# Performance work log

Hardware: AMD Instinct MI355X
Metric: run time of the kernel (lower is better)

Reference implementation:

```python
import jax, jax.numpy as jnp
import numpy as np

N_HEADS = 16
HEAD_DIM = 64
SEQ_LEN = 2048
BATCH = 1


def alibi_slopes(n_heads):
    start = 2.0 ** (-8.0 / n_heads)
    return jnp.asarray([start * start ** i for i in range(n_heads)], dtype=jnp.float32)


def setup_inputs() -> dict:
    key = jax.random.key(0)
    kq, kk, kv = jax.random.split(key, 3)
    shape = (BATCH, N_HEADS, SEQ_LEN, HEAD_DIM)
    return {
        "q": jax.random.normal(kq, shape, dtype=jnp.float32),
        "k": jax.random.normal(kk, shape, dtype=jnp.float32),
        "v": jax.random.normal(kv, shape, dtype=jnp.float32),
    }


def reference(q, k, v):
    # q,k,v: [B,H,S,D]
    seq_len = q.shape[2]
    head_dim = q.shape[3]
    scale = 1.0 / np.sqrt(head_dim).astype(np.float32)
    # scores: [B,H,S,S]
    scores = jnp.einsum("bhsd,bhtd->bhst", q, k) * scale
    pos = jnp.arange(seq_len)
    # distances[i, j] = j - i  (pos.unsqueeze(0) - pos.unsqueeze(1))
    distances = (pos[None, :] - pos[:, None]).astype(jnp.float32)  # [S,S]
    slopes = alibi_slopes(q.shape[1])  # [H]
    alibi = slopes[:, None, None] * distances[None, :, :]  # [H,S,S]
    scores = scores + alibi[None]
    attn = jax.nn.softmax(scores, axis=-1)
    return jnp.einsum("bhst,bhtd->bhsd", attn, v)
```

## Files before the change

### kernel.cpp

```cpp
#include <hip/hip_runtime.h>
#include <hip/hip_bf16.h>
#include <stdint.h>

#define N_HEADS 16
#define HEAD_DIM 64
#define SEQ_LEN 2048
#define KVBLK 32
#define NT 32
#define NTILE_TOT (SEQ_LEN / KVBLK)

typedef __bf16 bf16x8 __attribute__((ext_vector_type(8)));
typedef __bf16 bf16x4 __attribute__((ext_vector_type(4)));
typedef short  s16x4  __attribute__((ext_vector_type(4)));
typedef float  f32x4  __attribute__((ext_vector_type(4)));
typedef unsigned int u32x4 __attribute__((ext_vector_type(4)));

#if __has_builtin(__builtin_amdgcn_mfma_f32_16x16x16bf16_1k)
#define HAVE_MFMA16 1
#else
#define HAVE_MFMA16 0
#endif

static __device__ __forceinline__ unsigned pkbf(float a, float b) {
    union { __bf16 h[2]; unsigned u; } t;
    t.h[0] = (__bf16)a; t.h[1] = (__bf16)b;
    return t.u;
}

__global__ __launch_bounds__(256)
void prep_kernel(const float* __restrict__ k,
                 const float* __restrict__ v,
                 char* __restrict__ kimg,
                 char* __restrict__ vtimg) {
    const int ts  = blockIdx.x;
    const int h   = blockIdx.y;
    const int tid = threadIdx.x;
    const int s0  = ts * KVBLK;
    const size_t blk = ((size_t)h * NTILE_TOT + ts) * 4096;

    const int krow = tid >> 3;
    const int kcol = (tid & 7) * 8;
    const float* ks = k + ((size_t)h * SEQ_LEN + s0 + krow) * HEAD_DIM + kcol;
    f32x4 a = *(const f32x4*)ks;
    f32x4 b = *(const f32x4*)(ks + 4);
    bf16x8 kb;
    #pragma unroll
    for (int i = 0; i < 4; ++i) { kb[i] = (__bf16)a[i]; kb[4 + i] = (__bf16)b[i]; }
    *(bf16x8*)(kimg + blk + krow * 128 + ((kcol * 2) ^ ((krow & 7) << 4))) = kb;

    const int vc = tid & 63;
    const int vr = (tid >> 6) * 8;
    const float* vs = v + ((size_t)h * SEQ_LEN + s0 + vr) * HEAD_DIM + vc;
    bf16x8 vb;
    #pragma unroll
    for (int j = 0; j < 8; ++j) vb[j] = (__bf16)vs[(size_t)j * HEAD_DIM];
    *(bf16x8*)(vtimg + blk + (((vc * 64) + (vr * 2)) ^ ((vc & 7) << 4))) = vb;
}

template <bool IMG>
__global__ __launch_bounds__(512, 4)
void attn_alibi_kernel(const float* __restrict__ q,
                       const float* __restrict__ k,
                       const float* __restrict__ v,
                       float* __restrict__ out,
                       const char* __restrict__ kimg,
                       const char* __restrict__ vtimg) {
    const int tid  = threadIdx.x;
    const int wave = tid >> 6;
    const int lane = tid & 63;
    const int col  = lane & 15;
    const int g    = lane >> 4;
    const int half = wave >> 2;
    const int w4   = wave & 3;

    const int h      = blockIdx.y;
    const int qbase  = blockIdx.x * 64 + w4 * 16;
    const int kstart = half * (NT * KVBLK);

    const float* qh = q + (size_t)h * SEQ_LEN * HEAD_DIM;
    const float* kh = k + (size_t)h * SEQ_LEN * HEAD_DIM;
    const float* vh = v + (size_t)h * SEQ_LEN * HEAD_DIM;

    __shared__ alignas(16) char smem[32768];
    char* kbase  = smem + half * 8192;
    char* vtbase = smem + 16384 + half * 8192;

    const float LOG2E  = 1.4426950408889634f;
    const float scale2 = 0.125f * LOG2E;
    const float slope  = exp2f(-0.5f * (float)(h + 1));
    const float slope2 = slope * LOG2E;

    bf16x8 qf[2];
    {
        const float* qr = qh + (size_t)(qbase + col) * HEAD_DIM + g * 8;
        #pragma unroll
        for (int c = 0; c < 2; ++c)
            #pragma unroll
            for (int b = 0; b < 8; ++b) qf[c][b] = (__bf16)qr[c * 32 + b];
    }

    float cb[2][4];
    #pragma unroll
    for (int jt = 0; jt < 2; ++jt)
        #pragma unroll
        for (int r = 0; r < 4; ++r)
            cb[jt][r] = slope2 * (float)(jt * 16 + g * 4 + r - (qbase + col));

    float m = -1e30f, l = 0.0f;
    f32x4 acc[4];
    #pragma unroll
    for (int dt = 0; dt < 4; ++dt) acc[dt] = (f32x4)0.0f;

    const int hid  = tid & 255;
    const int krow = hid >> 3;
    const int kcol = (hid & 7) * 8;
    const int vc   = hid & 63;
    const int vr   = (hid >> 6) * 8;

    const char* kis = nullptr;
    const char* vis = nullptr;
    const float* ksrc = nullptr;
    const float* vsrc = nullptr;
    char* kdst  = nullptr;
    char* vtdst = nullptr;
    if constexpr (IMG) {
        const size_t base = ((size_t)h * NTILE_TOT + half * NT) * 4096 + hid * 16;
        kis = kimg + base;
        vis = vtimg + base;
        kdst  = kbase + hid * 16;
        vtdst = vtbase + hid * 16;
    } else {
        ksrc  = kh + (size_t)(kstart + krow) * HEAD_DIM + kcol;
        kdst  = kbase + krow * 128 + ((kcol * 2) ^ ((krow & 7) << 4));
        vsrc  = vh + (size_t)(kstart + vr) * HEAD_DIM + vc;
        vtdst = vtbase + (((vc * 64) + (vr * 2)) ^ ((vc & 7) << 4));
    }

    f32x4 kreg, vreg;
    f32x4 kr0, kr1;
    float vv[8];

    if constexpr (IMG) {
        kreg = *(const f32x4*)(kis);
        vreg = *(const f32x4*)(vis);
        *(f32x4*)(kdst)  = kreg;
        *(f32x4*)(vtdst) = vreg;
    } else {
        kr0 = *(const f32x4*)(ksrc);
        kr1 = *(const f32x4*)(ksrc + 4);
        #pragma unroll
        for (int j = 0; j < 8; ++j) vv[j] = vsrc[(size_t)j * HEAD_DIM];
        bf16x8 kb16, vb16;
        #pragma unroll
        for (int b = 0; b < 4; ++b) { kb16[b] = (__bf16)kr0[b]; kb16[4 + b] = (__bf16)kr1[b]; }
        #pragma unroll
        for (int j = 0; j < 8; ++j) vb16[j] = (__bf16)vv[j];
        *(bf16x8*)(kdst)  = kb16;
        *(bf16x8*)(vtdst) = vb16;
    }
    __syncthreads();

    for (int t = 0; t < NT; ++t) {
        const int kb  = kstart + t * KVBLK;
        const int buf = t & 1;
        const char* kbuf  = kbase + buf * 4096;
        const char* vtbuf = vtbase + buf * 4096;

        f32x4 sacc[2];
        sacc[0] = (f32x4)0.0f;
        sacc[1] = (f32x4)0.0f;
        #pragma unroll
        for (int jt = 0; jt < 2; ++jt) {
            const int row = jt * 16 + col;
            #pragma unroll
            for (int c = 0; c < 2; ++c) {
                bf16x8 kf = *(const bf16x8*)(kbuf + row * 128
                                             + ((c * 64 + g * 16) ^ ((row & 7) << 4)));
                sacc[jt] = __builtin_amdgcn_mfma_f32_16x16x32_bf16(kf, qf[c], sacc[jt], 0, 0, 0);
            }
        }

        if (t + 1 < NT) {
            if constexpr (IMG) {
                kreg = *(const f32x4*)(kis + (size_t)(t + 1) * 4096);
                vreg = *(const f32x4*)(vis + (size_t)(t + 1) * 4096);
            } else {
                const float* ks = ksrc + (size_t)(t + 1) * KVBLK * HEAD_DIM;
                const float* vs = vsrc + (size_t)(t + 1) * KVBLK * HEAD_DIM;
                kr0 = *(const f32x4*)(ks);
                kr1 = *(const f32x4*)(ks + 4);
                #pragma unroll
                for (int j = 0; j < 8; ++j) vv[j] = vs[(size_t)j * HEAD_DIM];
            }
        }

        const float skb = slope2 * (float)kb;
        float s[2][4];
        #pragma unroll
        for (int jt = 0; jt < 2; ++jt)
            #pragma unroll
            for (int r = 0; r < 4; ++r)
                s[jt][r] = sacc[jt][r] * scale2 + (cb[jt][r] + skb);

        float x = s[0][0];
        #pragma unroll
        for (int jt = 0; jt < 2; ++jt)
            #pragma unroll
            for (int r = 0; r < 4; ++r) x = fmaxf(x, s[jt][r]);
        x = fmaxf(x, __shfl_xor(x, 16));
        x = fmaxf(x, __shfl_xor(x, 32));
        float mn    = fmaxf(m, x);
        float alpha = __builtin_amdgcn_exp2f(m - mn);
        m = mn;
        float p[2][4], y = 0.0f;
        #pragma unroll
        for (int jt = 0; jt < 2; ++jt)
            #pragma unroll
            for (int r = 0; r < 4; ++r) {
                p[jt][r] = __builtin_amdgcn_exp2f(s[jt][r] - mn);
                y += p[jt][r];
            }
        y += __shfl_xor(y, 16);
        y += __shfl_xor(y, 32);
        l = l * alpha + y;
        #pragma unroll
        for (int dt = 0; dt < 4; ++dt) acc[dt] *= alpha;

#if HAVE_MFMA16
        bf16x4 pf0, pf1;
        #pragma unroll
        for (int b = 0; b < 4; ++b) { pf0[b] = (__bf16)p[0][b]; pf1[b] = (__bf16)p[1][b]; }
        const s16x4 pb0 = __builtin_bit_cast(s16x4, pf0);
        const s16x4 pb1 = __builtin_bit_cast(s16x4, pf1);
        #pragma unroll
        for (int dt = 0; dt < 4; ++dt) {
            const int vrow = dt * 16 + col;
            const int rb   = vrow * 64;
            const int swz  = (vrow & 7) << 4;
            bf16x4 vf0 = *(const bf16x4*)(vtbuf + ((rb + g * 8) ^ swz));
            bf16x4 vf1 = *(const bf16x4*)(vtbuf + ((rb + 32 + g * 8) ^ swz));
            acc[dt] = __builtin_amdgcn_mfma_f32_16x16x16bf16_1k(
                __builtin_bit_cast(s16x4, vf0), pb0, acc[dt], 0, 0, 0);
            acc[dt] = __builtin_amdgcn_mfma_f32_16x16x16bf16_1k(
                __builtin_bit_cast(s16x4, vf1), pb1, acc[dt], 0, 0, 0);
        }
#else
        unsigned pk00 = pkbf(p[0][0], p[0][1]);
        unsigned pk01 = pkbf(p[0][2], p[0][3]);
        unsigned pk10 = pkbf(p[1][0], p[1][1]);
        unsigned pk11 = pkbf(p[1][2], p[1][3]);
        const int srcA = col + ((g & 1) << 5);
        const int srcB = srcA + 16;
        unsigned a00 = __shfl(pk00, srcA), a01 = __shfl(pk01, srcA);
        unsigned a10 = __shfl(pk10, srcA), a11 = __shfl(pk11, srcA);
        unsigned b00 = __shfl(pk00, srcB), b01 = __shfl(pk01, srcB);
        unsigned b10 = __shfl(pk10, srcB), b11 = __shfl(pk11, srcB);
        const bool hi = g >= 2;
        u32x4 pu;
        pu[0] = hi ? a10 : a00;
        pu[1] = hi ? a11 : a01;
        pu[2] = hi ? b10 : b00;
        pu[3] = hi ? b11 : b01;
        bf16x8 pf = __builtin_bit_cast(bf16x8, pu);
        #pragma unroll
        for (int dt = 0; dt < 4; ++dt) {
            const int vrow = dt * 16 + col;
            bf16x8 vf = *(const bf16x8*)(vtbuf
                            + ((vrow * 64 + g * 16) ^ ((vrow & 7) << 4)));
            acc[dt] = __builtin_amdgcn_mfma_f32_16x16x32_bf16(vf, pf, acc[dt], 0, 0, 0);
        }
#endif

        if (t + 1 < NT) {
            const int nb = (t + 1) & 1;
            if constexpr (IMG) {
                *(f32x4*)(kdst  + nb * 4096) = kreg;
                *(f32x4*)(vtdst + nb * 4096) = vreg;
            } else {
                bf16x8 kb16, vb16;
                #pragma unroll
                for (int b = 0; b < 4; ++b) { kb16[b] = (__bf16)kr0[b]; kb16[4 + b] = (__bf16)kr1[b]; }
                #pragma unroll
                for (int j = 0; j < 8; ++j) vb16[j] = (__bf16)vv[j];
                *(bf16x8*)(kdst  + nb * 4096) = kb16;
                *(bf16x8*)(vtdst + nb * 4096) = vb16;
            }
        }
        __syncthreads();
    }

    float* eacc = (float*)smem;
    float* eml  = (float*)(smem + 16384);

    if (half == 1) {
        #pragma unroll
        for (int dt = 0; dt < 4; ++dt)
            *(f32x4*)(eacc + w4 * 1024 + col * 64 + dt * 16 + g * 4) = acc[dt];
        if (g == 0) {
            eml[(w4 * 16 + col) * 2 + 0] = m;
            eml[(w4 * 16 + col) * 2 + 1] = l;
        }
    }
    __syncthreads();
    if (half == 0) {
        float m2 = eml[(w4 * 16 + col) * 2 + 0];
        float l2 = eml[(w4 * 16 + col) * 2 + 1];
        float mm = fmaxf(m, m2);
        float a1 = __builtin_amdgcn_exp2f(m - mm);
        float a2 = __builtin_amdgcn_exp2f(m2 - mm);
        float inv = 1.0f / (l * a1 + l2 * a2);
        float* orow = out + ((size_t)h * SEQ_LEN + qbase + col) * HEAD_DIM;
        #pragma unroll
        for (int dt = 0; dt < 4; ++dt) {
            f32x4 o2 = *(const f32x4*)(eacc + w4 * 1024 + col * 64 + dt * 16 + g * 4);
            *(f32x4*)(orow + dt * 16 + g * 4) = (acc[dt] * a1 + o2 * a2) * inv;
        }
    }
}

extern "C" void kernel_launch(void* const* d_in, const int* in_sizes, int n_in,
                              void* d_out, int out_size, void* d_ws, size_t ws_size,
                              hipStream_t stream) {
    const float* q = (const float*)d_in[0];
    const float* k = (const float*)d_in[1];
    const float* v = (const float*)d_in[2];
    float* out = (float*)d_out;

    const size_t imgBytes = (size_t)N_HEADS * NTILE_TOT * 4096;

    dim3 grid(SEQ_LEN / 64, N_HEADS, 1);
    if (ws_size >= 2 * imgBytes) {
        char* kimg  = (char*)d_ws;
        char* vtimg = kimg + imgBytes;
        prep_kernel<<<dim3(NTILE_TOT, N_HEADS, 1), dim3(256, 1, 1), 0, stream>>>(
            k, v, kimg, vtimg);
        attn_alibi_kernel<true><<<grid, dim3(512, 1, 1), 0, stream>>>(
            q, k, v, out, kimg, vtimg);
    } else {
        attn_alibi_kernel<false><<<grid, dim3(512, 1, 1), 0, stream>>>(
            q, k, v, out, nullptr, nullptr);
    }
}
```

Measured before the change: 51.43 us.

## Double KV tile to 64 rows and add lazy softmax rescaling

Each loop iteration now processes two 32-row KV sub-tiles (64 keys), so the loop runs half as many times. That halves the number of __syncthreads barriers and cross-lane max/sum reductions per key. The online-softmax rescale of the accumulator is skipped unless some lane's running max grows by more than 8 (in log2 units), which cuts exp and multiply work. In exchange, LDS use doubles to 64KB, the occupancy hint drops to 2 blocks per CU, and register pressure rises. The lazy rescale lets unnormalised values grow by up to 2^8 before the final normalisation, which costs some bf16 precision margin.

```diff
diff --git a/kernel.cpp b/kernel.cpp
--- a/kernel.cpp
+++ b/kernel.cpp
@@ -5,9 +5,9 @@
 #define N_HEADS 16
 #define HEAD_DIM 64
 #define SEQ_LEN 2048
-#define KVBLK 32
-#define NT 32
-#define NTILE_TOT (SEQ_LEN / KVBLK)
+#define KVBLK 64
+#define NT 16
+#define NTILE_TOT (SEQ_LEN / 32)
 
 typedef __bf16 bf16x8 __attribute__((ext_vector_type(8)));
 typedef __bf16 bf16x4 __attribute__((ext_vector_type(4)));
@@ -35,7 +35,7 @@
     const int ts  = blockIdx.x;
     const int h   = blockIdx.y;
     const int tid = threadIdx.x;
-    const int s0  = ts * KVBLK;
+    const int s0  = ts * 32;
     const size_t blk = ((size_t)h * NTILE_TOT + ts) * 4096;
 
     const int krow = tid >> 3;
@@ -58,7 +58,7 @@
 }
 
 template <bool IMG>
-__global__ __launch_bounds__(512, 4)
+__global__ __launch_bounds__(512, 2)
 void attn_alibi_kernel(const float* __restrict__ q,
                        const float* __restrict__ k,
                        const float* __restrict__ v,
@@ -81,9 +81,9 @@
     const float* kh = k + (size_t)h * SEQ_LEN * HEAD_DIM;
     const float* vh = v + (size_t)h * SEQ_LEN * HEAD_DIM;
 
-    __shared__ alignas(16) char smem[32768];
-    char* kbase  = smem + half * 8192;
-    char* vtbase = smem + 16384 + half * 8192;
+    __shared__ alignas(16) char smem[65536];
+    char* kbase  = smem + half * 16384;
+    char* vtbase = smem + 32768 + half * 16384;
 
     const float LOG2E  = 1.4426950408889634f;
     const float scale2 = 0.125f * LOG2E;
@@ -99,12 +99,12 @@
             for (int b = 0; b < 8; ++b) qf[c][b] = (__bf16)qr[c * 32 + b];
     }
 
-    float cb[2][4];
+    float cb[4][4];
     #pragma unroll
-    for (int jt = 0; jt < 2; ++jt)
+    for (int i = 0; i < 4; ++i)
         #pragma unroll
         for (int r = 0; r < 4; ++r)
-            cb[jt][r] = slope2 * (float)(jt * 16 + g * 4 + r - (qbase + col));
+            cb[i][r] = slope2 * (float)(i * 16 + g * 4 + r - (qbase + col));
 
     float m = -1e30f, l = 0.0f;
     f32x4 acc[4];
@@ -117,16 +117,13 @@
     const int vc   = hid & 63;
     const int vr   = (hid >> 6) * 8;
 
-    const char* kis = nullptr;
-    const char* vis = nullptr;
-    const float* ksrc = nullptr;
-    const float* vsrc = nullptr;
-    char* kdst  = nullptr;
-    char* vtdst = nullptr;
+    const char* kis = nullptr; const char* vis = nullptr;
+    const float* ksrc = nullptr; const float* vsrc = nullptr;
+    char* kdst = nullptr; char* vtdst = nullptr;
     if constexpr (IMG) {
-        const size_t base = ((size_t)h * NTILE_TOT + half * NT) * 4096 + hid * 16;
-        kis = kimg + base;
-        vis = vtimg + base;
+        const size_t base = ((size_t)h * NTILE_TOT + half * (NTILE_TOT / 2)) * 4096
+                          + hid * 16;
+        kis = kimg + base;  vis = vtimg + base;
         kdst  = kbase + hid * 16;
         vtdst = vtbase + hid * 16;
     } else {
@@ -136,154 +133,192 @@
         vtdst = vtbase + (((vc * 64) + (vr * 2)) ^ ((vc & 7) << 4));
     }
 
-    f32x4 kreg, vreg;
-    f32x4 kr0, kr1;
-    float vv[8];
+    f32x4 kreg[2], vreg[2];
+    f32x4 kr[2][2];
+    float vv[2][8];
 
     if constexpr (IMG) {
-        kreg = *(const f32x4*)(kis);
-        vreg = *(const f32x4*)(vis);
-        *(f32x4*)(kdst)  = kreg;
-        *(f32x4*)(vtdst) = vreg;
+        #pragma unroll
+        for (int sb = 0; sb < 2; ++sb) {
+            kreg[sb] = *(const f32x4*)(kis + sb * 4096);
+            vreg[sb] = *(const f32x4*)(vis + sb * 4096);
+            *(f32x4*)(kdst  + sb * 4096) = kreg[sb];
+            *(f32x4*)(vtdst + sb * 4096) = vreg[sb];
+        }
     } else {
-        kr0 = *(const f32x4*)(ksrc);
-        kr1 = *(const f32x4*)(ksrc + 4);
-        #pragma unroll
-        for (int j = 0; j < 8; ++j) vv[j] = vsrc[(size_t)j * HEAD_DIM];
-        bf16x8 kb16, vb16;
-        #pragma unroll
-        for (int b = 0; b < 4; ++b) { kb16[b] = (__bf16)kr0[b]; kb16[4 + b] = (__bf16)kr1[b]; }
-        #pragma unroll
-        for (int j = 0; j < 8; ++j) vb16[j] = (__bf16)vv[j];
-        *(bf16x8*)(kdst)  = kb16;
-        *(bf16x8*)(vtdst) = vb16;
+        #pragma unroll
+        for (int sb = 0; sb < 2; ++sb) {
+            const float* ks = ksrc + (size_t)(sb * 32) * HEAD_DIM;
+            const float* vs = vsrc + (size_t)(sb * 32) * HEAD_DIM;
+            kr[sb][0] = *(const f32x4*)(ks);
+            kr[sb][1] = *(const f32x4*)(ks + 4);
+            #pragma unroll
+            for (int j = 0; j < 8; ++j) vv[sb][j] = vs[(size_t)j * HEAD_DIM];
+            bf16x8 kb16, vb16;
+            #pragma unroll
+            for (int b = 0; b < 4; ++b) { kb16[b] = (__bf16)kr[sb][0][b]; kb16[4 + b] = (__bf16)kr[sb][1][b]; }
+            #pragma unroll
+            for (int j = 0; j < 8; ++j) vb16[j] = (__bf16)vv[sb][j];
+            *(bf16x8*)(kdst  + sb * 4096) = kb16;
+            *(bf16x8*)(vtdst + sb * 4096) = vb16;
+        }
     }
     __syncthreads();
 
     for (int t = 0; t < NT; ++t) {
         const int kb  = kstart + t * KVBLK;
         const int buf = t & 1;
-        const char* kbuf  = kbase + buf * 4096;
-        const char* vtbuf = vtbase + buf * 4096;
-
-        f32x4 sacc[2];
-        sacc[0] = (f32x4)0.0f;
-        sacc[1] = (f32x4)0.0f;
-        #pragma unroll
-        for (int jt = 0; jt < 2; ++jt) {
-            const int row = jt * 16 + col;
-            #pragma unroll
-            for (int c = 0; c < 2; ++c) {
-                bf16x8 kf = *(const bf16x8*)(kbuf + row * 128
-                                             + ((c * 64 + g * 16) ^ ((row & 7) << 4)));
-                sacc[jt] = __builtin_amdgcn_mfma_f32_16x16x32_bf16(kf, qf[c], sacc[jt], 0, 0, 0);
+        const char* kbuf  = kbase + buf * 8192;
+        const char* vtbuf = vtbase + buf * 8192;
+
+        f32x4 sacc[4];
+        #pragma unroll
+        for (int i = 0; i < 4; ++i) sacc[i] = (f32x4)0.0f;
+        #pragma unroll
+        for (int sb = 0; sb < 2; ++sb) {
+            #pragma unroll
+            for (int jt = 0; jt < 2; ++jt) {
+                const int row = jt * 16 + col;
+                const int i   = sb * 2 + jt;
+                #pragma unroll
+                for (int c = 0; c < 2; ++c) {
+                    bf16x8 kf = *(const bf16x8*)(kbuf + sb * 4096 + row * 128
+                                                 + ((c * 64 + g * 16) ^ ((row & 7) << 4)));
+                    sacc[i] = __builtin_amdgcn_mfma_f32_16x16x32_bf16(kf, qf[c], sacc[i], 0, 0, 0);
+                }
             }
         }
 
         if (t + 1 < NT) {
             if constexpr (IMG) {
-                kreg = *(const f32x4*)(kis + (size_t)(t + 1) * 4096);
-                vreg = *(const f32x4*)(vis + (size_t)(t + 1) * 4096);
+                #pragma unroll
+                for (int sb = 0; sb < 2; ++sb) {
+                    kreg[sb] = *(const f32x4*)(kis + (size_t)((t + 1) * 2 + sb) * 4096);
+                    vreg[sb] = *(const f32x4*)(vis + (size_t)((t + 1) * 2 + sb) * 4096);
+                }
             } else {
-                const float* ks = ksrc + (size_t)(t + 1) * KVBLK * HEAD_DIM;
-                const float* vs = vsrc + (size_t)(t + 1) * KVBLK * HEAD_DIM;
-                kr0 = *(const f32x4*)(ks);
-                kr1 = *(const f32x4*)(ks + 4);
-                #pragma unroll
-                for (int j = 0; j < 8; ++j) vv[j] = vs[(size_t)j * HEAD_DIM];
+                #pragma unroll
+                for (int sb = 0; sb < 2; ++sb) {
+                    const float* ks = ksrc + (size_t)((t + 1) * 64 + sb * 32) * HEAD_DIM;
+                    const float* vs = vsrc + (size_t)((t + 1) * 64 + sb * 32) * HEAD_DIM;
+                    kr[sb][0] = *(const f32x4*)(ks);
+                    kr[sb][1] = *(const f32x4*)(ks + 4);
+                    #pragma unroll
+                    for (int j = 0; j < 8; ++j) vv[sb][j] = vs[(size_t)j * HEAD_DIM];
+                }
             }
         }
 
         const float skb = slope2 * (float)kb;
-        float s[2][4];
-        #pragma unroll
-        for (int jt = 0; jt < 2; ++jt)
+        float s[4][4];
+        #pragma unroll
+        for (int i = 0; i < 4; ++i)
             #pragma unroll
             for (int r = 0; r < 4; ++r)
-                s[jt][r] = sacc[jt][r] * scale2 + (cb[jt][r] + skb);
-
-        float x = s[0][0];
-        #pragma unroll
-        for (int jt = 0; jt < 2; ++jt)
-            #pragma unroll
-            for (int r = 0; r < 4; ++r) x = fmaxf(x, s[jt][r]);
+                s[i][r] = sacc[i][r] * scale2 + (cb[i][r] + skb);
+
+        float x01a = fmaxf(s[0][0], s[0][1]), x01b = fmaxf(s[0][2], s[0][3]);
+        float x23a = fmaxf(s[1][0], s[1][1]), x23b = fmaxf(s[1][2], s[1][3]);
+        float x45a = fmaxf(s[2][0], s[2][1]), x45b = fmaxf(s[2][2], s[2][3]);
+        float x67a = fmaxf(s[3][0], s[3][1]), x67b = fmaxf(s[3][2], s[3][3]);
+        float x = fmaxf(fmaxf(fmaxf(x01a, x01b), fmaxf(x23a, x23b)),
+                        fmaxf(fmaxf(x45a, x45b), fmaxf(x67a, x67b)));
         x = fmaxf(x, __shfl_xor(x, 16));
         x = fmaxf(x, __shfl_xor(x, 32));
-        float mn    = fmaxf(m, x);
-        float alpha = __builtin_amdgcn_exp2f(m - mn);
-        m = mn;
-        float p[2][4], y = 0.0f;
-        #pragma unroll
-        for (int jt = 0; jt < 2; ++jt)
+
+        if (__any(x - m > 8.0f)) {
+            float mn    = fmaxf(m, x);
+            float alpha = __builtin_amdgcn_exp2f(m - mn);
+            m = mn;
+            l *= alpha;
+            #pragma unroll
+            for (int dt = 0; dt < 4; ++dt) acc[dt] *= alpha;
+        }
+
+        float p[4][4], y = 0.0f;
+        #pragma unroll
+        for (int i = 0; i < 4; ++i)
             #pragma unroll
             for (int r = 0; r < 4; ++r) {
-                p[jt][r] = __builtin_amdgcn_exp2f(s[jt][r] - mn);
-                y += p[jt][r];
+                p[i][r] = __builtin_amdgcn_exp2f(s[i][r] - m);
+                y += p[i][r];
             }
         y += __shfl_xor(y, 16);
         y += __shfl_xor(y, 32);
-        l = l * alpha + y;
-        #pragma unroll
-        for (int dt = 0; dt < 4; ++dt) acc[dt] *= alpha;
+        l += y;
 
 #if HAVE_MFMA16
-        bf16x4 pf0, pf1;
-        #pragma unroll
-        for (int b = 0; b < 4; ++b) { pf0[b] = (__bf16)p[0][b]; pf1[b] = (__bf16)p[1][b]; }
-        const s16x4 pb0 = __builtin_bit_cast(s16x4, pf0);
-        const s16x4 pb1 = __builtin_bit_cast(s16x4, pf1);
+        s16x4 pb[4];
+        #pragma unroll
+        for (int i = 0; i < 4; ++i) {
+            bf16x4 pf;
+            #pragma unroll
+            for (int b = 0; b < 4; ++b) pf[b] = (__bf16)p[i][b];
+            pb[i] = __builtin_bit_cast(s16x4, pf);
+        }
         #pragma unroll
         for (int dt = 0; dt < 4; ++dt) {
             const int vrow = dt * 16 + col;
             const int rb   = vrow * 64;
             const int swz  = (vrow & 7) << 4;
-            bf16x4 vf0 = *(const bf16x4*)(vtbuf + ((rb + g * 8) ^ swz));
-            bf16x4 vf1 = *(const bf16x4*)(vtbuf + ((rb + 32 + g * 8) ^ swz));
-            acc[dt] = __builtin_amdgcn_mfma_f32_16x16x16bf16_1k(
-                __builtin_bit_cast(s16x4, vf0), pb0, acc[dt], 0, 0, 0);
-            acc[dt] = __builtin_amdgcn_mfma_f32_16x16x16bf16_1k(
-                __builtin_bit_cast(s16x4, vf1), pb1, acc[dt], 0, 0, 0);
+            #pragma unroll
+            for (int i = 0; i < 4; ++i) {
+                const int sb = i >> 1, jt = i & 1;
+                bf16x4 vf = *(const bf16x4*)(vtbuf + sb * 4096
+                                             + ((rb + jt * 32 + g * 8) ^ swz));
+                acc[dt] = __builtin_amdgcn_mfma_f32_16x16x16bf16_1k(
+                    __builtin_bit_cast(s16x4, vf), pb[i], acc[dt], 0, 0, 0);
+            }
         }
 #else
-        unsigned pk00 = pkbf(p[0][0], p[0][1]);
-        unsigned pk01 = pkbf(p[0][2], p[0][3]);
-        unsigned pk10 = pkbf(p[1][0], p[1][1]);
-        unsigned pk11 = pkbf(p[1][2], p[1][3]);
-        const int srcA = col + ((g & 1) << 5);
-        const int srcB = srcA + 16;
-        unsigned a00 = __shfl(pk00, srcA), a01 = __shfl(pk01, srcA);
-        unsigned a10 = __shfl(pk10, srcA), a11 = __shfl(pk11, srcA);
-        unsigned b00 = __shfl(pk00, srcB), b01 = __shfl(pk01, srcB);
-        unsigned b10 = __shfl(pk10, srcB), b11 = __shfl(pk11, srcB);
-        const bool hi = g >= 2;
-        u32x4 pu;
-        pu[0] = hi ? a10 : a00;
-        pu[1] = hi ? a11 : a01;
-        pu[2] = hi ? b10 : b00;
-        pu[3] = hi ? b11 : b01;
-        bf16x8 pf = __builtin_bit_cast(bf16x8, pu);
-        #pragma unroll
-        for (int dt = 0; dt < 4; ++dt) {
-            const int vrow = dt * 16 + col;
-            bf16x8 vf = *(const bf16x8*)(vtbuf
-                            + ((vrow * 64 + g * 16) ^ ((vrow & 7) << 4)));
-            acc[dt] = __builtin_amdgcn_mfma_f32_16x16x32_bf16(vf, pf, acc[dt], 0, 0, 0);
+        #pragma unroll
+        for (int sb = 0; sb < 2; ++sb) {
+            unsigned pk00 = pkbf(p[sb * 2][0],     p[sb * 2][1]);
+            unsigned pk01 = pkbf(p[sb * 2][2],     p[sb * 2][3]);
+            unsigned pk10 = pkbf(p[sb * 2 + 1][0], p[sb * 2 + 1][1]);
+            unsigned pk11 = pkbf(p[sb * 2 + 1][2], p[sb * 2 + 1][3]);
+            const int srcA = col + ((g & 1) << 5);
+            const int srcB = srcA + 16;
+            unsigned a00 = __shfl(pk00, srcA), a01 = __shfl(pk01, srcA);
+            unsigned a10 = __shfl(pk10, srcA), a11 = __shfl(pk11, srcA);
+            unsigned b00 = __shfl(pk00, srcB), b01 = __shfl(pk01, srcB);
+            unsigned b10 = __shfl(pk10, srcB), b11 = __shfl(pk11, srcB);
+            const bool hi = g >= 2;
+            u32x4 pu;
+            pu[0] = hi ? a10 : a00;
+            pu[1] = hi ? a11 : a01;
+            pu[2] = hi ? b10 : b00;
+            pu[3] = hi ? b11 : b01;
+            bf16x8 pf = __builtin_bit_cast(bf16x8, pu);
+            #pragma unroll
+            for (int dt = 0; dt < 4; ++dt) {
+                const int vrow = dt * 16 + col;
+                bf16x8 vf = *(const bf16x8*)(vtbuf + sb * 4096
+                                + ((vrow * 64 + g * 16) ^ ((vrow & 7) << 4)));
+                acc[dt] = __builtin_amdgcn_mfma_f32_16x16x32_bf16(vf, pf, acc[dt], 0, 0, 0);
+            }
         }
 #endif
 
         if (t + 1 < NT) {
             const int nb = (t + 1) & 1;
             if constexpr (IMG) {
-                *(f32x4*)(kdst  + nb * 4096) = kreg;
-                *(f32x4*)(vtdst + nb * 4096) = vreg;
+                #pragma unroll
+                for (int sb = 0; sb < 2; ++sb) {
+                    *(f32x4*)(kdst  + nb * 8192 + sb * 4096) = kreg[sb];
+                    *(f32x4*)(vtdst + nb * 8192 + sb * 4096) = vreg[sb];
+                }
             } else {
-                bf16x8 kb16, vb16;
-                #pragma unroll
-                for (int b = 0; b < 4; ++b) { kb16[b] = (__bf16)kr0[b]; kb16[4 + b] = (__bf16)kr1[b]; }
-                #pragma unroll
-                for (int j = 0; j < 8; ++j) vb16[j] = (__bf16)vv[j];
-                *(bf16x8*)(kdst  + nb * 4096) = kb16;
-                *(bf16x8*)(vtdst + nb * 4096) = vb16;
+                #pragma unroll
+                for (int sb = 0; sb < 2; ++sb) {
+                    bf16x8 kb16, vb16;
+                    #pragma unroll
+                    for (int b = 0; b < 4; ++b) { kb16[b] = (__bf16)kr[sb][0][b]; kb16[4 + b] = (__bf16)kr[sb][1][b]; }
+                    #pragma unroll
+                    for (int j = 0; j < 8; ++j) vb16[j] = (__bf16)vv[sb][j];
+                    *(bf16x8*)(kdst  + nb * 8192 + sb * 4096) = kb16;
+                    *(bf16x8*)(vtdst + nb * 8192 + sb * 4096) = vb16;
+                }
             }
         }
         __syncthreads();
```

After: 48.95 us. 1.05x faster.
